# Performance work log

Hardware: AMD Instinct MI355X
Metric: run time of the kernel (lower is better)

The kernel has to match this reference:

```python
import jax, jax.numpy as jnp
import numpy as np

N_UNITS = 100000
N_EDGES = 1600000
NODE_DIM = 64
N_REL_TYPES = 8
LEAKY_SLOPE = 0.2


def setup_inputs() -> dict:
    key = jax.random.key(0)
    k1, k2, k3, k4, k5 = jax.random.split(key, 5)
    x_unit_base = jax.random.normal(k1, (N_UNITS, NODE_DIM), dtype=jnp.float32)
    hat_t = jax.random.normal(k2, (N_UNITS,), dtype=jnp.float32)
    a_r_params = jax.random.normal(k3, (N_REL_TYPES, 2 * NODE_DIM), dtype=jnp.float32)
    rel_edge_index = jax.random.randint(k4, (2, N_EDGES), 0, N_UNITS, dtype=jnp.int64)
    rel_edge_type = jax.random.randint(k5, (N_EDGES,), 0, N_REL_TYPES, dtype=jnp.int64)
    return {
        "x_unit_base": x_unit_base,
        "hat_t": hat_t,
        "a_r_params": a_r_params,
        "rel_edge_index": rel_edge_index,
        "rel_edge_type": rel_edge_type,
    }


def reference(x_unit_base, hat_t, a_r_params, rel_edge_index, rel_edge_type):
    n_units = x_unit_base.shape[0]
    src = rel_edge_index[0]  # [E]
    dst = rel_edge_index[1]  # [E]

    # Per-edge attention params, split into source/dest halves to avoid
    # materializing the [E, 2d] concat explicitly as a separate buffer.
    a_r = a_r_params[rel_edge_type]          # [E, 2d]
    d = x_unit_base.shape[1]
    a_u, a_v = a_r[:, :d], a_r[:, d:]
    # e = sum(a_r * cat(x_u, x_v)) = <a_u, x_u> + <a_v, x_v>
    e = jnp.sum(a_u * x_unit_base[src], axis=-1) + jnp.sum(a_v * x_unit_base[dst], axis=-1)
    e = jax.nn.leaky_relu(e, negative_slope=LEAKY_SLOPE)  # [E]

    # scatter_softmax over edges grouped by src
    seg_max = jax.ops.segment_max(e, src, num_segments=n_units)  # [N]
    ex = jnp.exp(e - seg_max[src])
    denom = jax.ops.segment_sum(ex, src, num_segments=n_units)   # [N]
    alpha = ex / denom[src]                                       # [E]

    # weighted scatter-sum of imputed treatments
    weighted_t = alpha * hat_t[dst]
    g_u = jax.ops.segment_sum(weighted_t, src, num_segments=n_units)  # [N]
    return g_u[:, None]
```

## Files before the change

### kernel.cpp

```cpp
#include <hip/hip_runtime.h>

#define LEAKY_SLOPE 0.2f
#define SHIFT 20.0f
#define CHUNK 2048
#define LG_CHUNK 11
#define NG 8
#define NSL 2
#define NB_MAX 512
#define EPB 4096
#define CAP_MIN 4608


__device__ __forceinline__ float lrelu_exp(float a, float b) {
    float e = a + b;
    e = (e > 0.f) ? e : LEAKY_SLOPE * e;
    return __expf(e - SHIFT);
}

__global__ __launch_bounds__(256) void table_scatter_kernel(
        const float* __restrict__ x, const float* __restrict__ a,
        const float* __restrict__ hat_t,
        const int* __restrict__ src, const int* __restrict__ dst,
        const int* __restrict__ typ,
        float* __restrict__ su, float* __restrict__ svx,
        unsigned* __restrict__ gcur, unsigned* __restrict__ buckets,
        int cap, int nch, int n_units, int n_edges, int gs) {
    __shared__ unsigned lcnt[NB_MAX];
    __shared__ unsigned lbase[NB_MAX];
    const int tid = threadIdx.x;

    if ((int)blockIdx.x < gs) {
        const int nb = nch * NG;
        for (int i = tid; i < nb; i += 256) lcnt[i] = 0u;
        __syncthreads();

        const int base = blockIdx.x * EPB;
        unsigned ent[16], rnk[16], bkt[16];
#pragma unroll
        for (int r = 0; r < 4; ++r) {
            int e = base + tid * 4 + r * 1024;
            if (e + 4 <= n_edges) {
                int4 s4 = *reinterpret_cast<const int4*>(src + e);
                int4 d4 = *reinterpret_cast<const int4*>(dst + e);
                int4 t4 = *reinterpret_cast<const int4*>(typ + e);
                int ss[4] = {s4.x, s4.y, s4.z, s4.w};
                int dd[4] = {d4.x, d4.y, d4.z, d4.w};
                int tt[4] = {t4.x, t4.y, t4.z, t4.w};
#pragma unroll
                for (int i = 0; i < 4; ++i) {
                    unsigned s = (unsigned)ss[i], d = (unsigned)dd[i], t = (unsigned)tt[i];
                    unsigned b = (s >> LG_CHUNK) * NG + ((d >> LG_CHUNK) & (NG - 1));
                    ent[r * 4 + i] = ((s & (CHUNK - 1)) << 21) | (t << 18) | d;
                    bkt[r * 4 + i] = b;
                    rnk[r * 4 + i] = atomicAdd(&lcnt[b], 1u);
                }
            } else {
#pragma unroll
                for (int i = 0; i < 4; ++i) {
                    int ee = e + i;
                    if (ee < n_edges) {
                        unsigned s = (unsigned)src[ee], d = (unsigned)dst[ee], t = (unsigned)typ[ee];
                        unsigned b = (s >> LG_CHUNK) * NG + ((d >> LG_CHUNK) & (NG - 1));
                        ent[r * 4 + i] = ((s & (CHUNK - 1)) << 21) | (t << 18) | d;
                        bkt[r * 4 + i] = b;
                        rnk[r * 4 + i] = atomicAdd(&lcnt[b], 1u);
                    } else {
                        bkt[r * 4 + i] = 0xFFFFFFFFu;
                    }
                }
            }
        }
        __syncthreads();
        for (int i = tid; i < nb; i += 256)
            lbase[i] = lcnt[i] ? atomicAdd(&gcur[i], lcnt[i]) : 0u;
        __syncthreads();
#pragma unroll
        for (int k = 0; k < 16; ++k) {
            unsigned b = bkt[k];
            if (b != 0xFFFFFFFFu) {
                unsigned pos = lbase[b] + rnk[k];
                if (pos < (unsigned)cap)
                    buckets[(size_t)b * cap + pos] = ent[k];
            }
        }
    } else {
        int u = ((int)blockIdx.x - gs) * 256 + tid;
        if (u >= n_units) return;
        float4 xr[16];
        const float4* xp = reinterpret_cast<const float4*>(x + (size_t)u * 64);
#pragma unroll
        for (int k = 0; k < 16; ++k) xr[k] = xp[k];

        float out_u[8], out_v[8];
#pragma unroll
        for (int r = 0; r < 8; ++r) {
            const float* ar = a + r * 128;
            float au = 0.f, av = 0.f;
#pragma unroll
            for (int k = 0; k < 16; ++k) {
                float4 xk = xr[k];
                au = fmaf(ar[4 * k + 0], xk.x, au);
                au = fmaf(ar[4 * k + 1], xk.y, au);
                au = fmaf(ar[4 * k + 2], xk.z, au);
                au = fmaf(ar[4 * k + 3], xk.w, au);
                av = fmaf(ar[64 + 4 * k + 0], xk.x, av);
                av = fmaf(ar[64 + 4 * k + 1], xk.y, av);
                av = fmaf(ar[64 + 4 * k + 2], xk.z, av);
                av = fmaf(ar[64 + 4 * k + 3], xk.w, av);
            }
            out_u[r] = au;
            out_v[r] = av;
        }
        float4* sup = reinterpret_cast<float4*>(su + (size_t)u * 8);
        sup[0] = make_float4(out_u[0], out_u[1], out_u[2], out_u[3]);
        sup[1] = make_float4(out_u[4], out_u[5], out_u[6], out_u[7]);
        float ht = hat_t[u];
        float4* svp = reinterpret_cast<float4*>(svx + (size_t)u * 16);
        svp[0] = make_float4(out_v[0], ht, out_v[1], ht);
        svp[1] = make_float4(out_v[2], ht, out_v[3], ht);
        svp[2] = make_float4(out_v[4], ht, out_v[5], ht);
        svp[3] = make_float4(out_v[6], ht, out_v[7], ht);
    }
}

__device__ __forceinline__ void accum_edge(unsigned e, const float* __restrict__ suc,
                                           const float2* __restrict__ svh,
                                           float* __restrict__ lden,
                                           float* __restrict__ lnum) {
    unsigned s_l = e >> 21;
    unsigned t = (e >> 18) & 7u;
    unsigned d = e & 0x3FFFFu;
    float suv = suc[(s_l << 3) | t];
    float2 pv = svh[((size_t)d << 3) | t];
    float ex = lrelu_exp(suv, pv.x);
    atomicAdd(&lden[s_l], ex);
    atomicAdd(&lnum[s_l], ex * pv.y);
}

__global__ __launch_bounds__(256) void accum_kernel(const unsigned* __restrict__ buckets,
                                                    const unsigned* __restrict__ gcur,
                                                    const float* __restrict__ su,
                                                    const float2* __restrict__ svh,
                                                    float2* __restrict__ partial,
                                                    int cap) {
    __shared__ float lden[CHUNK];
    __shared__ float lnum[CHUNK];
    const int bid = blockIdx.x;
    const int g = bid & (NG - 1);
    const int rest = bid >> 3;
    const int sl = rest & (NSL - 1);
    const int c = rest >> 1;
    for (int i = threadIdx.x; i < CHUNK; i += 256) { lden[i] = 0.f; lnum[i] = 0.f; }
    __syncthreads();

    const int b = c * NG + g;
    int cnt = (int)gcur[b];
    if (cnt > cap) cnt = cap;
    const unsigned* ep = buckets + (size_t)b * cap;
    int lo = (sl * cnt / NSL) & ~3;
    int hi = (sl == NSL - 1) ? cnt : (((sl + 1) * cnt / NSL) & ~3);
    const float* suc = su + (((size_t)c << LG_CHUNK) << 3);

    for (int i = lo + threadIdx.x * 4; i + 4 <= hi; i += 1024) {
        uint4 q = *reinterpret_cast<const uint4*>(ep + i);
        accum_edge(q.x, suc, svh, lden, lnum);
        accum_edge(q.y, suc, svh, lden, lnum);
        accum_edge(q.z, suc, svh, lden, lnum);
        accum_edge(q.w, suc, svh, lden, lnum);
    }
    int rem = (hi - lo) & 3;
    if ((int)threadIdx.x < rem) accum_edge(ep[hi - rem + threadIdx.x], suc, svh, lden, lnum);

    __syncthreads();
    float2* op = partial + (size_t)bid * CHUNK;
    for (int k = threadIdx.x; k < CHUNK; k += 256)
        op[k] = make_float2(lden[k], lnum[k]);
}

__global__ __launch_bounds__(256) void reduce_kernel(const float2* __restrict__ partial,
                                                     float* __restrict__ out,
                                                     int n_units) {
    int u = blockIdx.x * blockDim.x + threadIdx.x;
    if (u >= n_units) return;
    int c = u >> LG_CHUNK;
    int i = u & (CHUNK - 1);
    const float2* p = partial + ((size_t)c * (NSL * NG)) * CHUNK + i;
    float den = 0.f, num = 0.f;
#pragma unroll
    for (int k = 0; k < NSL * NG; ++k) {
        float2 v = p[(size_t)k * CHUNK];
        den += v.x;
        num += v.y;
    }
    out[u] = (den > 0.f) ? num / den : 0.f;
}

template <bool FUSED>
__global__ __launch_bounds__(256) void node_table_fb_kernel(const float* __restrict__ x,
                                                            const float* __restrict__ a,
                                                            const float* __restrict__ hat_t,
                                                            float* __restrict__ su,
                                                            float* __restrict__ svx,
                                                            float2* __restrict__ nd,
                                                            int n_units) {
    int u = blockIdx.x * blockDim.x + threadIdx.x;
    if (u >= n_units) return;
    nd[u] = make_float2(0.f, 0.f);
    float4 xr[16];
    const float4* xp = reinterpret_cast<const float4*>(x + (size_t)u * 64);
#pragma unroll
    for (int k = 0; k < 16; ++k) xr[k] = xp[k];
    float out_u[8], out_v[8];
#pragma unroll
    for (int r = 0; r < 8; ++r) {
        const float* ar = a + r * 128;
        float au = 0.f, av = 0.f;
#pragma unroll
        for (int k = 0; k < 16; ++k) {
            float4 xk = xr[k];
            au = fmaf(ar[4 * k + 0], xk.x, au);
            au = fmaf(ar[4 * k + 1], xk.y, au);
            au = fmaf(ar[4 * k + 2], xk.z, au);
            au = fmaf(ar[4 * k + 3], xk.w, au);
            av = fmaf(ar[64 + 4 * k + 0], xk.x, av);
            av = fmaf(ar[64 + 4 * k + 1], xk.y, av);
            av = fmaf(ar[64 + 4 * k + 2], xk.z, av);
            av = fmaf(ar[64 + 4 * k + 3], xk.w, av);
        }
        out_u[r] = au;
        out_v[r] = av;
    }
    float4* sup = reinterpret_cast<float4*>(su + (size_t)u * 8);
    sup[0] = make_float4(out_u[0], out_u[1], out_u[2], out_u[3]);
    sup[1] = make_float4(out_u[4], out_u[5], out_u[6], out_u[7]);
    if (FUSED) {
        float ht = hat_t[u];
        float4* svp = reinterpret_cast<float4*>(svx + (size_t)u * 16);
        svp[0] = make_float4(out_v[0], ht, out_v[1], ht);
        svp[1] = make_float4(out_v[2], ht, out_v[3], ht);
        svp[2] = make_float4(out_v[4], ht, out_v[5], ht);
        svp[3] = make_float4(out_v[6], ht, out_v[7], ht);
    } else {
        float4* svp = reinterpret_cast<float4*>(svx + (size_t)u * 8);
        svp[0] = make_float4(out_v[0], out_v[1], out_v[2], out_v[3]);
        svp[1] = make_float4(out_v[4], out_v[5], out_v[6], out_v[7]);
    }
}

__device__ __forceinline__ void pair_add_dev(float* f, float a, float b) {
    atomicAdd(f, a);
    atomicAdd(f + 1, b);
}

template <bool FUSED>
__global__ __launch_bounds__(256) void edge_sum_kernel(const int* __restrict__ src,
                                                       const int* __restrict__ dst,
                                                       const int* __restrict__ typ,
                                                       const float* __restrict__ su,
                                                       const float* __restrict__ svx,
                                                       const float* __restrict__ hat_t,
                                                       float2* __restrict__ nd,
                                                       int n_edges) {
    int e0 = (blockIdx.x * blockDim.x + threadIdx.x) * 2;
    float* ndf = (float*)nd;
    if (e0 + 1 < n_edges) {
        int2 s2 = *reinterpret_cast<const int2*>(src + e0);
        int2 d2 = *reinterpret_cast<const int2*>(dst + e0);
        int2 t2 = *reinterpret_cast<const int2*>(typ + e0);
        float su0 = su[(size_t)s2.x * 8 + t2.x];
        float su1 = su[(size_t)s2.y * 8 + t2.y];
        float sv0, sv1, ht0, ht1;
        if (FUSED) {
            const float2* svh = reinterpret_cast<const float2*>(svx);
            float2 p0 = svh[(size_t)d2.x * 8 + t2.x];
            float2 p1 = svh[(size_t)d2.y * 8 + t2.y];
            sv0 = p0.x; ht0 = p0.y;
            sv1 = p1.x; ht1 = p1.y;
        } else {
            sv0 = svx[(size_t)d2.x * 8 + t2.x];
            sv1 = svx[(size_t)d2.y * 8 + t2.y];
            ht0 = hat_t[d2.x];
            ht1 = hat_t[d2.y];
        }
        float ex0 = lrelu_exp(su0, sv0);
        float ex1 = lrelu_exp(su1, sv1);
        pair_add_dev(ndf + 2 * (size_t)s2.x, ex0, ex0 * ht0);
        pair_add_dev(ndf + 2 * (size_t)s2.y, ex1, ex1 * ht1);
    } else if (e0 < n_edges) {
        int s = src[e0], d = dst[e0], t = typ[e0];
        float sv_v, ht;
        if (FUSED) {
            float2 p = reinterpret_cast<const float2*>(svx)[(size_t)d * 8 + t];
            sv_v = p.x; ht = p.y;
        } else {
            sv_v = svx[(size_t)d * 8 + t];
            ht = hat_t[d];
        }
        float ex = lrelu_exp(su[(size_t)s * 8 + t], sv_v);
        pair_add_dev(ndf + 2 * (size_t)s, ex, ex * ht);
    }
}

__global__ __launch_bounds__(256) void finalize_kernel(const float2* __restrict__ nd,
                                                       float* __restrict__ out, int n) {
    int i = blockIdx.x * blockDim.x + threadIdx.x;
    if (i < n) {
        float2 v = nd[i];
        out[i] = (v.x > 0.f) ? v.y / v.x : 0.f;
    }
}

extern "C" void kernel_launch(void* const* d_in, const int* in_sizes, int n_in,
                              void* d_out, int out_size, void* d_ws, size_t ws_size,
                              hipStream_t stream) {
    const float* x     = (const float*)d_in[0];
    const float* hat_t = (const float*)d_in[1];
    const float* a     = (const float*)d_in[2];
    const int*   ei    = (const int*)d_in[3];
    const int*   et    = (const int*)d_in[4];

    const int n_units = in_sizes[1];
    const int n_edges = in_sizes[4];
    const int* src = ei;
    const int* dst = ei + n_edges;

    const size_t n = (size_t)n_units;
    const int B = 256;
    const int gu = (n_units + B - 1) / B;
    char* ws = (char*)d_ws;

    const int nch = (n_units + CHUNK - 1) >> LG_CHUNK;
    const int nb = nch * NG;
    const size_t tab = n * 96;
    const size_t curb = 4096;
    const size_t partb = (size_t)nch * NSL * NG * CHUNK * 8;

    int cap = 0;
    if (nb <= NB_MAX && n_units < (1 << 18)) {
        size_t head = tab + curb + partb;
        if (ws_size > head) {
            cap = (int)((ws_size - head) / ((size_t)nb * 4)) & ~3;
            if (cap > 8192) cap = 8192;
            if (cap < CAP_MIN) cap = 0;
        }
    }

    if (cap > 0) {
        float* su       = (float*)ws;
        float* svx      = su + n * 8;
        unsigned* gcur  = (unsigned*)(ws + tab);
        unsigned* buckets = (unsigned*)(ws + tab + curb);
        float2* partial = (float2*)(ws + tab + curb + (size_t)nb * cap * 4);
        const int gs = (n_edges + EPB - 1) / EPB;

        hipMemsetAsync(gcur, 0, (size_t)nb * 4, stream);
        table_scatter_kernel<<<gs + gu, B, 0, stream>>>(x, a, hat_t, src, dst, et,
                                                        su, svx, gcur, buckets,
                                                        cap, nch, n_units, n_edges, gs);
        accum_kernel<<<nch * NSL * NG, B, 0, stream>>>(buckets, gcur, su,
                                                       (const float2*)svx, partial, cap);
        reduce_kernel<<<gu, B, 0, stream>>>(partial, (float*)d_out, n_units);
    } else if (ws_size >= n * 104) {
        float2* nd = (float2*)ws;
        float* su  = (float*)(ws + n * 8);
        float* svx = su + n * 8;
        const int ge = ((n_edges + 1) / 2 + B - 1) / B;
        node_table_fb_kernel<true><<<gu, B, 0, stream>>>(x, a, hat_t, su, svx, nd, n_units);
        edge_sum_kernel<true><<<ge, B, 0, stream>>>(src, dst, et, su, svx, hat_t, nd, n_edges);
        finalize_kernel<<<gu, B, 0, stream>>>(nd, (float*)d_out, n_units);
    } else {
        float2* nd = (float2*)ws;
        float* su  = (float*)(ws + n * 8);
        float* svx = su + n * 8;
        const int ge = ((n_edges + 1) / 2 + B - 1) / B;
        node_table_fb_kernel<false><<<gu, B, 0, stream>>>(x, a, hat_t, su, svx, nd, n_units);
        edge_sum_kernel<false><<<ge, B, 0, stream>>>(src, dst, et, su, svx, hat_t, nd, n_edges);
        finalize_kernel<<<gu, B, 0, stream>>>(nd, (float*)d_out, n_units);
    }
}
```

Before: 138.3 us.

## Stage bucket scatter through shared memory and drop accum slice split

Result: no change. 137.1 us (-0.9%).

```diff
diff --git a/kernel.cpp b/kernel.cpp
--- a/kernel.cpp
+++ b/kernel.cpp
@@ -5,8 +5,8 @@
 #define CHUNK 2048
 #define LG_CHUNK 11
 #define NG 8
-#define NSL 2
 #define NB_MAX 512
+#define NB_PAD 512
 #define EPB 4096
 #define CAP_MIN 4608
 
@@ -25,13 +25,16 @@
         float* __restrict__ su, float* __restrict__ svx,
         unsigned* __restrict__ gcur, unsigned* __restrict__ buckets,
         int cap, int nch, int n_units, int n_edges, int gs) {
-    __shared__ unsigned lcnt[NB_MAX];
-    __shared__ unsigned lbase[NB_MAX];
+    __shared__ unsigned cnt[NB_PAD];
+    __shared__ unsigned sA[NB_PAD];
+    __shared__ unsigned sB[NB_PAD];
+    __shared__ unsigned sent[EPB];
+    __shared__ unsigned short sbk[EPB];
     const int tid = threadIdx.x;
 
     if ((int)blockIdx.x < gs) {
         const int nb = nch * NG;
-        for (int i = tid; i < nb; i += 256) lcnt[i] = 0u;
+        for (int i = tid; i < NB_PAD; i += 256) cnt[i] = 0u;
         __syncthreads();
 
         const int base = blockIdx.x * EPB;
@@ -52,7 +55,7 @@
                     unsigned b = (s >> LG_CHUNK) * NG + ((d >> LG_CHUNK) & (NG - 1));
                     ent[r * 4 + i] = ((s & (CHUNK - 1)) << 21) | (t << 18) | d;
                     bkt[r * 4 + i] = b;
-                    rnk[r * 4 + i] = atomicAdd(&lcnt[b], 1u);
+                    rnk[r * 4 + i] = atomicAdd(&cnt[b], 1u);
                 }
             } else {
 #pragma unroll
@@ -63,7 +66,7 @@
                         unsigned b = (s >> LG_CHUNK) * NG + ((d >> LG_CHUNK) & (NG - 1));
                         ent[r * 4 + i] = ((s & (CHUNK - 1)) << 21) | (t << 18) | d;
                         bkt[r * 4 + i] = b;
-                        rnk[r * 4 + i] = atomicAdd(&lcnt[b], 1u);
+                        rnk[r * 4 + i] = atomicAdd(&cnt[b], 1u);
                     } else {
                         bkt[r * 4 + i] = 0xFFFFFFFFu;
                     }
@@ -71,17 +74,39 @@
             }
         }
         __syncthreads();
-        for (int i = tid; i < nb; i += 256)
-            lbase[i] = lcnt[i] ? atomicAdd(&gcur[i], lcnt[i]) : 0u;
-        __syncthreads();
+        {
+            for (int i = tid; i < NB_PAD; i += 256)
+                sA[i] = cnt[i] + (i >= 1 ? cnt[i - 1] : 0u);
+            __syncthreads();
+            unsigned* pin = sA;
+            unsigned* pout = sB;
+#pragma unroll
+            for (int off = 2; off < NB_PAD; off <<= 1) {
+                for (int i = tid; i < NB_PAD; i += 256)
+                    pout[i] = pin[i] + (i >= off ? pin[i - off] : 0u);
+                __syncthreads();
+                unsigned* t2 = pin; pin = pout; pout = t2;
+            }
+        }
 #pragma unroll
         for (int k = 0; k < 16; ++k) {
             unsigned b = bkt[k];
             if (b != 0xFFFFFFFFu) {
-                unsigned pos = lbase[b] + rnk[k];
-                if (pos < (unsigned)cap)
-                    buckets[(size_t)b * cap + pos] = ent[k];
+                unsigned slot = (b ? sA[b - 1] : 0u) + rnk[k];
+                sent[slot] = ent[k];
+                sbk[slot] = (unsigned short)b;
             }
+        }
+        __syncthreads();
+        for (int b = tid; b < nb; b += 256)
+            sB[b] = cnt[b] ? atomicAdd(&gcur[b], cnt[b]) : 0u;
+        const int stot = (int)sA[nb - 1];
+        __syncthreads();
+        for (int i = tid; i < stot; i += 256) {
+            unsigned b = sbk[i];
+            unsigned pos = sB[b] + ((unsigned)i - (b ? sA[b - 1] : 0u));
+            if (pos < (unsigned)cap)
+                buckets[(size_t)b * cap + pos] = sent[i];
         }
     } else {
         int u = ((int)blockIdx.x - gs) * 256 + tid;
@@ -147,9 +172,7 @@
     __shared__ float lnum[CHUNK];
     const int bid = blockIdx.x;
     const int g = bid & (NG - 1);
-    const int rest = bid >> 3;
-    const int sl = rest & (NSL - 1);
-    const int c = rest >> 1;
+    const int c = bid >> 3;
     for (int i = threadIdx.x; i < CHUNK; i += 256) { lden[i] = 0.f; lnum[i] = 0.f; }
     __syncthreads();
 
@@ -157,19 +180,17 @@
     int cnt = (int)gcur[b];
     if (cnt > cap) cnt = cap;
     const unsigned* ep = buckets + (size_t)b * cap;
-    int lo = (sl * cnt / NSL) & ~3;
-    int hi = (sl == NSL - 1) ? cnt : (((sl + 1) * cnt / NSL) & ~3);
     const float* suc = su + (((size_t)c << LG_CHUNK) << 3);
 
-    for (int i = lo + threadIdx.x * 4; i + 4 <= hi; i += 1024) {
+    for (int i = threadIdx.x * 4; i + 4 <= cnt; i += 1024) {
         uint4 q = *reinterpret_cast<const uint4*>(ep + i);
         accum_edge(q.x, suc, svh, lden, lnum);
         accum_edge(q.y, suc, svh, lden, lnum);
         accum_edge(q.z, suc, svh, lden, lnum);
         accum_edge(q.w, suc, svh, lden, lnum);
     }
-    int rem = (hi - lo) & 3;
-    if ((int)threadIdx.x < rem) accum_edge(ep[hi - rem + threadIdx.x], suc, svh, lden, lnum);
+    int rem = cnt & 3;
+    if ((int)threadIdx.x < rem) accum_edge(ep[cnt - rem + threadIdx.x], suc, svh, lden, lnum);
 
     __syncthreads();
     float2* op = partial + (size_t)bid * CHUNK;
@@ -184,10 +205,10 @@
     if (u >= n_units) return;
     int c = u >> LG_CHUNK;
     int i = u & (CHUNK - 1);
-    const float2* p = partial + ((size_t)c * (NSL * NG)) * CHUNK + i;
+    const float2* p = partial + ((size_t)c * NG) * CHUNK + i;
     float den = 0.f, num = 0.f;
 #pragma unroll
-    for (int k = 0; k < NSL * NG; ++k) {
+    for (int k = 0; k < NG; ++k) {
         float2 v = p[(size_t)k * CHUNK];
         den += v.x;
         num += v.y;
@@ -333,7 +354,7 @@
     const int nb = nch * NG;
     const size_t tab = n * 96;
     const size_t curb = 4096;
-    const size_t partb = (size_t)nch * NSL * NG * CHUNK * 8;
+    const size_t partb = (size_t)nb * CHUNK * 8;
 
     int cap = 0;
     if (nb <= NB_MAX && n_units < (1 << 18)) {
@@ -357,8 +378,8 @@
         table_scatter_kernel<<<gs + gu, B, 0, stream>>>(x, a, hat_t, src, dst, et,
                                                         su, svx, gcur, buckets,
                                                         cap, nch, n_units, n_edges, gs);
-        accum_kernel<<<nch * NSL * NG, B, 0, stream>>>(buckets, gcur, su,
-                                                       (const float2*)svx, partial, cap);
+        accum_kernel<<<nb, B, 0, stream>>>(buckets, gcur, su,
+                                           (const float2*)svx, partial, cap);
         reduce_kernel<<<gu, B, 0, stream>>>(partial, (float*)d_out, n_units);
     } else if (ws_size >= n * 104) {
         float2* nd = (float2*)ws;
```

## Fuse scatter, accumulate and reduce into one cooperative persistent kernel

Applied to the files above, without the earlier changes.

After: 325.3 us. 2.35x slower.

```diff
diff --git a/kernel.cpp b/kernel.cpp
--- a/kernel.cpp
+++ b/kernel.cpp
@@ -1,4 +1,7 @@
 #include <hip/hip_runtime.h>
+#include <hip/hip_cooperative_groups.h>
+
+namespace cg = cooperative_groups;
 
 #define LEAKY_SLOPE 0.2f
 #define SHIFT 20.0f
@@ -6,7 +9,7 @@
 #define LG_CHUNK 11
 #define NG 8
 #define NSL 2
-#define NB_MAX 512
+#define NB_PAD 512
 #define EPB 4096
 #define CAP_MIN 4608
 
@@ -15,112 +18,6 @@
     float e = a + b;
     e = (e > 0.f) ? e : LEAKY_SLOPE * e;
     return __expf(e - SHIFT);
-}
-
-__global__ __launch_bounds__(256) void table_scatter_kernel(
-        const float* __restrict__ x, const float* __restrict__ a,
-        const float* __restrict__ hat_t,
-        const int* __restrict__ src, const int* __restrict__ dst,
-        const int* __restrict__ typ,
-        float* __restrict__ su, float* __restrict__ svx,
-        unsigned* __restrict__ gcur, unsigned* __restrict__ buckets,
-        int cap, int nch, int n_units, int n_edges, int gs) {
-    __shared__ unsigned lcnt[NB_MAX];
-    __shared__ unsigned lbase[NB_MAX];
-    const int tid = threadIdx.x;
-
-    if ((int)blockIdx.x < gs) {
-        const int nb = nch * NG;
-        for (int i = tid; i < nb; i += 256) lcnt[i] = 0u;
-        __syncthreads();
-
-        const int base = blockIdx.x * EPB;
-        unsigned ent[16], rnk[16], bkt[16];
-#pragma unroll
-        for (int r = 0; r < 4; ++r) {
-            int e = base + tid * 4 + r * 1024;
-            if (e + 4 <= n_edges) {
-                int4 s4 = *reinterpret_cast<const int4*>(src + e);
-                int4 d4 = *reinterpret_cast<const int4*>(dst + e);
-                int4 t4 = *reinterpret_cast<const int4*>(typ + e);
-                int ss[4] = {s4.x, s4.y, s4.z, s4.w};
-                int dd[4] = {d4.x, d4.y, d4.z, d4.w};
-                int tt[4] = {t4.x, t4.y, t4.z, t4.w};
-#pragma unroll
-                for (int i = 0; i < 4; ++i) {
-                    unsigned s = (unsigned)ss[i], d = (unsigned)dd[i], t = (unsigned)tt[i];
-                    unsigned b = (s >> LG_CHUNK) * NG + ((d >> LG_CHUNK) & (NG - 1));
-                    ent[r * 4 + i] = ((s & (CHUNK - 1)) << 21) | (t << 18) | d;
-                    bkt[r * 4 + i] = b;
-                    rnk[r * 4 + i] = atomicAdd(&lcnt[b], 1u);
-                }
-            } else {
-#pragma unroll
-                for (int i = 0; i < 4; ++i) {
-                    int ee = e + i;
-                    if (ee < n_edges) {
-                        unsigned s = (unsigned)src[ee], d = (unsigned)dst[ee], t = (unsigned)typ[ee];
-                        unsigned b = (s >> LG_CHUNK) * NG + ((d >> LG_CHUNK) & (NG - 1));
-                        ent[r * 4 + i] = ((s & (CHUNK - 1)) << 21) | (t << 18) | d;
-                        bkt[r * 4 + i] = b;
-                        rnk[r * 4 + i] = atomicAdd(&lcnt[b], 1u);
-                    } else {
-                        bkt[r * 4 + i] = 0xFFFFFFFFu;
-                    }
-                }
-            }
-        }
-        __syncthreads();
-        for (int i = tid; i < nb; i += 256)
-            lbase[i] = lcnt[i] ? atomicAdd(&gcur[i], lcnt[i]) : 0u;
-        __syncthreads();
-#pragma unroll
-        for (int k = 0; k < 16; ++k) {
-            unsigned b = bkt[k];
-            if (b != 0xFFFFFFFFu) {
-                unsigned pos = lbase[b] + rnk[k];
-                if (pos < (unsigned)cap)
-                    buckets[(size_t)b * cap + pos] = ent[k];
-            }
-        }
-    } else {
-        int u = ((int)blockIdx.x - gs) * 256 + tid;
-        if (u >= n_units) return;
-        float4 xr[16];
-        const float4* xp = reinterpret_cast<const float4*>(x + (size_t)u * 64);
-#pragma unroll
-        for (int k = 0; k < 16; ++k) xr[k] = xp[k];
-
-        float out_u[8], out_v[8];
-#pragma unroll
-        for (int r = 0; r < 8; ++r) {
-            const float* ar = a + r * 128;
-            float au = 0.f, av = 0.f;
-#pragma unroll
-            for (int k = 0; k < 16; ++k) {
-                float4 xk = xr[k];
-                au = fmaf(ar[4 * k + 0], xk.x, au);
-                au = fmaf(ar[4 * k + 1], xk.y, au);
-                au = fmaf(ar[4 * k + 2], xk.z, au);
-                au = fmaf(ar[4 * k + 3], xk.w, au);
-                av = fmaf(ar[64 + 4 * k + 0], xk.x, av);
-                av = fmaf(ar[64 + 4 * k + 1], xk.y, av);
-                av = fmaf(ar[64 + 4 * k + 2], xk.z, av);
-                av = fmaf(ar[64 + 4 * k + 3], xk.w, av);
-            }
-            out_u[r] = au;
-            out_v[r] = av;
-        }
-        float4* sup = reinterpret_cast<float4*>(su + (size_t)u * 8);
-        sup[0] = make_float4(out_u[0], out_u[1], out_u[2], out_u[3]);
-        sup[1] = make_float4(out_u[4], out_u[5], out_u[6], out_u[7]);
-        float ht = hat_t[u];
-        float4* svp = reinterpret_cast<float4*>(svx + (size_t)u * 16);
-        svp[0] = make_float4(out_v[0], ht, out_v[1], ht);
-        svp[1] = make_float4(out_v[2], ht, out_v[3], ht);
-        svp[2] = make_float4(out_v[4], ht, out_v[5], ht);
-        svp[3] = make_float4(out_v[6], ht, out_v[7], ht);
-    }
 }
 
 __device__ __forceinline__ void accum_edge(unsigned e, const float* __restrict__ suc,
@@ -137,62 +34,174 @@
     atomicAdd(&lnum[s_l], ex * pv.y);
 }
 
-__global__ __launch_bounds__(256) void accum_kernel(const unsigned* __restrict__ buckets,
-                                                    const unsigned* __restrict__ gcur,
-                                                    const float* __restrict__ su,
-                                                    const float2* __restrict__ svh,
-                                                    float2* __restrict__ partial,
-                                                    int cap) {
-    __shared__ float lden[CHUNK];
-    __shared__ float lnum[CHUNK];
+__global__ __launch_bounds__(256, 4) void fused_kernel(
+        const float* __restrict__ x, const float* __restrict__ a,
+        const float* __restrict__ hat_t,
+        const int* __restrict__ src, const int* __restrict__ dst,
+        const int* __restrict__ typ,
+        float* __restrict__ su, float* __restrict__ svx,
+        unsigned* __restrict__ gcur, unsigned* __restrict__ buckets,
+        float2* __restrict__ partial, float* __restrict__ out,
+        int cap, int nch, int n_units, int n_edges, int gs, int gu) {
+    __shared__ float lds[2 * CHUNK];
+    cg::grid_group grid = cg::this_grid();
+    const int tid = threadIdx.x;
     const int bid = blockIdx.x;
-    const int g = bid & (NG - 1);
-    const int rest = bid >> 3;
-    const int sl = rest & (NSL - 1);
-    const int c = rest >> 1;
-    for (int i = threadIdx.x; i < CHUNK; i += 256) { lden[i] = 0.f; lnum[i] = 0.f; }
-    __syncthreads();
-
-    const int b = c * NG + g;
-    int cnt = (int)gcur[b];
-    if (cnt > cap) cnt = cap;
-    const unsigned* ep = buckets + (size_t)b * cap;
-    int lo = (sl * cnt / NSL) & ~3;
-    int hi = (sl == NSL - 1) ? cnt : (((sl + 1) * cnt / NSL) & ~3);
-    const float* suc = su + (((size_t)c << LG_CHUNK) << 3);
-
-    for (int i = lo + threadIdx.x * 4; i + 4 <= hi; i += 1024) {
-        uint4 q = *reinterpret_cast<const uint4*>(ep + i);
-        accum_edge(q.x, suc, svh, lden, lnum);
-        accum_edge(q.y, suc, svh, lden, lnum);
-        accum_edge(q.z, suc, svh, lden, lnum);
-        accum_edge(q.w, suc, svh, lden, lnum);
-    }
-    int rem = (hi - lo) & 3;
-    if ((int)threadIdx.x < rem) accum_edge(ep[hi - rem + threadIdx.x], suc, svh, lden, lnum);
-
-    __syncthreads();
-    float2* op = partial + (size_t)bid * CHUNK;
-    for (int k = threadIdx.x; k < CHUNK; k += 256)
-        op[k] = make_float2(lden[k], lnum[k]);
-}
-
-__global__ __launch_bounds__(256) void reduce_kernel(const float2* __restrict__ partial,
-                                                     float* __restrict__ out,
-                                                     int n_units) {
-    int u = blockIdx.x * blockDim.x + threadIdx.x;
-    if (u >= n_units) return;
-    int c = u >> LG_CHUNK;
-    int i = u & (CHUNK - 1);
-    const float2* p = partial + ((size_t)c * (NSL * NG)) * CHUNK + i;
-    float den = 0.f, num = 0.f;
-#pragma unroll
-    for (int k = 0; k < NSL * NG; ++k) {
-        float2 v = p[(size_t)k * CHUNK];
-        den += v.x;
-        num += v.y;
-    }
-    out[u] = (den > 0.f) ? num / den : 0.f;
+    const int G = gridDim.x;
+    const int nb = nch * NG;
+
+    for (int i = bid * 256 + tid; i < nb; i += G * 256) gcur[i] = 0u;
+    grid.sync();
+
+    {
+        unsigned* lcnt = (unsigned*)lds;
+        unsigned* lbase = lcnt + NB_PAD;
+        for (int it = bid; it < gs + gu; it += G) {
+            if (it < gs) {
+                for (int i = tid; i < nb; i += 256) lcnt[i] = 0u;
+                __syncthreads();
+                const int base = it * EPB;
+                unsigned ent[16], rnk[16], bkt[16];
+#pragma unroll
+                for (int r = 0; r < 4; ++r) {
+                    int e = base + tid * 4 + r * 1024;
+                    if (e + 4 <= n_edges) {
+                        int4 s4 = *reinterpret_cast<const int4*>(src + e);
+                        int4 d4 = *reinterpret_cast<const int4*>(dst + e);
+                        int4 t4 = *reinterpret_cast<const int4*>(typ + e);
+                        int ss[4] = {s4.x, s4.y, s4.z, s4.w};
+                        int dd[4] = {d4.x, d4.y, d4.z, d4.w};
+                        int tt[4] = {t4.x, t4.y, t4.z, t4.w};
+#pragma unroll
+                        for (int i = 0; i < 4; ++i) {
+                            unsigned s = (unsigned)ss[i], d = (unsigned)dd[i], t = (unsigned)tt[i];
+                            unsigned b = (s >> LG_CHUNK) * NG + ((d >> LG_CHUNK) & (NG - 1));
+                            ent[r * 4 + i] = ((s & (CHUNK - 1)) << 21) | (t << 18) | d;
+                            bkt[r * 4 + i] = b;
+                            rnk[r * 4 + i] = atomicAdd(&lcnt[b], 1u);
+                        }
+                    } else {
+#pragma unroll
+                        for (int i = 0; i < 4; ++i) {
+                            int ee = e + i;
+                            if (ee < n_edges) {
+                                unsigned s = (unsigned)src[ee], d = (unsigned)dst[ee],
+                                         t = (unsigned)typ[ee];
+                                unsigned b = (s >> LG_CHUNK) * NG + ((d >> LG_CHUNK) & (NG - 1));
+                                ent[r * 4 + i] = ((s & (CHUNK - 1)) << 21) | (t << 18) | d;
+                                bkt[r * 4 + i] = b;
+                                rnk[r * 4 + i] = atomicAdd(&lcnt[b], 1u);
+                            } else {
+                                bkt[r * 4 + i] = 0xFFFFFFFFu;
+                            }
+                        }
+                    }
+                }
+                __syncthreads();
+                for (int i = tid; i < nb; i += 256)
+                    lbase[i] = lcnt[i] ? atomicAdd(&gcur[i], lcnt[i]) : 0u;
+                __syncthreads();
+#pragma unroll
+                for (int k = 0; k < 16; ++k) {
+                    unsigned b = bkt[k];
+                    if (b != 0xFFFFFFFFu) {
+                        unsigned pos = lbase[b] + rnk[k];
+                        if (pos < (unsigned)cap)
+                            buckets[(size_t)b * cap + pos] = ent[k];
+                    }
+                }
+                __syncthreads();
+            } else {
+                int u = (it - gs) * 256 + tid;
+                if (u < n_units) {
+                    float4 xr[16];
+                    const float4* xp = reinterpret_cast<const float4*>(x + (size_t)u * 64);
+#pragma unroll
+                    for (int k = 0; k < 16; ++k) xr[k] = xp[k];
+                    float out_u[8], out_v[8];
+#pragma unroll
+                    for (int r = 0; r < 8; ++r) {
+                        const float* ar = a + r * 128;
+                        float au = 0.f, av = 0.f;
+#pragma unroll
+                        for (int k = 0; k < 16; ++k) {
+                            float4 xk = xr[k];
+                            au = fmaf(ar[4 * k + 0], xk.x, au);
+                            au = fmaf(ar[4 * k + 1], xk.y, au);
+                            au = fmaf(ar[4 * k + 2], xk.z, au);
+                            au = fmaf(ar[4 * k + 3], xk.w, au);
+                            av = fmaf(ar[64 + 4 * k + 0], xk.x, av);
+                            av = fmaf(ar[64 + 4 * k + 1], xk.y, av);
+                            av = fmaf(ar[64 + 4 * k + 2], xk.z, av);
+                            av = fmaf(ar[64 + 4 * k + 3], xk.w, av);
+                        }
+                        out_u[r] = au;
+                        out_v[r] = av;
+                    }
+                    float4* sup = reinterpret_cast<float4*>(su + (size_t)u * 8);
+                    sup[0] = make_float4(out_u[0], out_u[1], out_u[2], out_u[3]);
+                    sup[1] = make_float4(out_u[4], out_u[5], out_u[6], out_u[7]);
+                    float ht = hat_t[u];
+                    float4* svp = reinterpret_cast<float4*>(svx + (size_t)u * 16);
+                    svp[0] = make_float4(out_v[0], ht, out_v[1], ht);
+                    svp[1] = make_float4(out_v[2], ht, out_v[3], ht);
+                    svp[2] = make_float4(out_v[4], ht, out_v[5], ht);
+                    svp[3] = make_float4(out_v[6], ht, out_v[7], ht);
+                }
+            }
+        }
+    }
+    grid.sync();
+
+    {
+        float* lden = lds;
+        float* lnum = lds + CHUNK;
+        const float2* svh = reinterpret_cast<const float2*>(svx);
+        for (int item = bid; item < nb * NSL; item += G) {
+            int g = item & (NG - 1);
+            int rest = item >> 3;
+            int sl = rest & (NSL - 1);
+            int c = rest >> 1;
+            for (int i = tid; i < CHUNK; i += 256) { lden[i] = 0.f; lnum[i] = 0.f; }
+            __syncthreads();
+            const int b = c * NG + g;
+            int cnt = (int)gcur[b];
+            if (cnt > cap) cnt = cap;
+            const unsigned* ep = buckets + (size_t)b * cap;
+            const float* suc = su + (((size_t)c << LG_CHUNK) << 3);
+            int lo = (sl * cnt / NSL) & ~3;
+            int hi = (sl == NSL - 1) ? cnt : (((sl + 1) * cnt / NSL) & ~3);
+            for (int i = lo + tid * 4; i + 4 <= hi; i += 1024) {
+                uint4 q = *reinterpret_cast<const uint4*>(ep + i);
+                accum_edge(q.x, suc, svh, lden, lnum);
+                accum_edge(q.y, suc, svh, lden, lnum);
+                accum_edge(q.z, suc, svh, lden, lnum);
+                accum_edge(q.w, suc, svh, lden, lnum);
+            }
+            int rem = (hi - lo) & 3;
+            if (tid < rem) accum_edge(ep[hi - rem + tid], suc, svh, lden, lnum);
+            __syncthreads();
+            float2* op = partial + (size_t)item * CHUNK;
+            for (int k = tid; k < CHUNK; k += 256)
+                op[k] = make_float2(lden[k], lnum[k]);
+            __syncthreads();
+        }
+    }
+    grid.sync();
+
+    for (int u = bid * 256 + tid; u < n_units; u += G * 256) {
+        int c = u >> LG_CHUNK;
+        int i = u & (CHUNK - 1);
+        const float2* p = partial + ((size_t)c * (NG * NSL)) * CHUNK + i;
+        float den = 0.f, num = 0.f;
+#pragma unroll
+        for (int k = 0; k < NG * NSL; ++k) {
+            float2 v = p[(size_t)k * CHUNK];
+            den += v.x;
+            num += v.y;
+        }
+        out[u] = (den > 0.f) ? num / den : 0.f;
+    }
 }
 
 template <bool FUSED>
@@ -333,10 +342,10 @@
     const int nb = nch * NG;
     const size_t tab = n * 96;
     const size_t curb = 4096;
-    const size_t partb = (size_t)nch * NSL * NG * CHUNK * 8;
+    const size_t partb = (size_t)nb * NSL * CHUNK * 8;
 
     int cap = 0;
-    if (nb <= NB_MAX && n_units < (1 << 18)) {
+    if (nb <= NB_PAD && n_units < (1 << 18)) {
         size_t head = tab + curb + partb;
         if (ws_size > head) {
             cap = (int)((ws_size - head) / ((size_t)nb * 4)) & ~3;
@@ -345,21 +354,34 @@
         }
     }
 
+    int G = 0;
     if (cap > 0) {
+        int dev = 0, ncu = 0, occ = 0;
+        hipGetDevice(&dev);
+        hipDeviceGetAttribute(&ncu, hipDeviceAttributeMultiprocessorCount, dev);
+        hipOccupancyMaxActiveBlocksPerMultiprocessor(&occ, fused_kernel, 256, 0);
+        G = occ * ncu;
+        if (G > 1024) G = 1024;
+        G &= ~7;
+    }
+
+    if (cap > 0 && G >= 8) {
         float* su       = (float*)ws;
         float* svx      = su + n * 8;
         unsigned* gcur  = (unsigned*)(ws + tab);
         unsigned* buckets = (unsigned*)(ws + tab + curb);
         float2* partial = (float2*)(ws + tab + curb + (size_t)nb * cap * 4);
+        float* outp     = (float*)d_out;
         const int gs = (n_edges + EPB - 1) / EPB;
 
-        hipMemsetAsync(gcur, 0, (size_t)nb * 4, stream);
-        table_scatter_kernel<<<gs + gu, B, 0, stream>>>(x, a, hat_t, src, dst, et,
-                                                        su, svx, gcur, buckets,
-                                                        cap, nch, n_units, n_edges, gs);
-        accum_kernel<<<nch * NSL * NG, B, 0, stream>>>(buckets, gcur, su,
-                                                       (const float2*)svx, partial, cap);
-        reduce_kernel<<<gu, B, 0, stream>>>(partial, (float*)d_out, n_units);
+        int nu = n_units, ne = n_edges, gsv = gs, guv = gu, capv = cap, nchv = nch;
+        void* args[] = {(void*)&x, (void*)&a, (void*)&hat_t,
+                        (void*)&src, (void*)&dst, (void*)&et,
+                        (void*)&su, (void*)&svx, (void*)&gcur, (void*)&buckets,
+                        (void*)&partial, (void*)&outp,
+                        (void*)&capv, (void*)&nchv, (void*)&nu, (void*)&ne,
+                        (void*)&gsv, (void*)&guv};
+        hipLaunchCooperativeKernel((void*)fused_kernel, dim3(G), dim3(B), args, 0, stream);
     } else if (ws_size >= n * 104) {
         float2* nd = (float2*)ws;
         float* su  = (float*)(ws + n * 8);
```

## Bucket edges by small source chunks and fuse accumulation with final division

Applied to the files above, without the earlier changes.

Measured after the change: 134.6 us, median of 2. 1.03x faster.

```diff
diff --git a/kernel.cpp b/kernel.cpp
--- a/kernel.cpp
+++ b/kernel.cpp
@@ -2,13 +2,10 @@
 
 #define LEAKY_SLOPE 0.2f
 #define SHIFT 20.0f
-#define CHUNK 2048
-#define LG_CHUNK 11
-#define NG 8
-#define NSL 2
-#define NB_MAX 512
+#define CHUNK 128
+#define LG_CHUNK 7
+#define NB_MAX 1024
 #define EPB 4096
-#define CAP_MIN 4608
 
 
 __device__ __forceinline__ float lrelu_exp(float a, float b) {
@@ -19,18 +16,16 @@
 
 __global__ __launch_bounds__(256) void table_scatter_kernel(
         const float* __restrict__ x, const float* __restrict__ a,
-        const float* __restrict__ hat_t,
         const int* __restrict__ src, const int* __restrict__ dst,
         const int* __restrict__ typ,
-        float* __restrict__ su, float* __restrict__ svx,
+        float* __restrict__ su, float* __restrict__ sv,
         unsigned* __restrict__ gcur, unsigned* __restrict__ buckets,
-        int cap, int nch, int n_units, int n_edges, int gs) {
-    __shared__ unsigned lcnt[NB_MAX];
-    __shared__ unsigned lbase[NB_MAX];
+        int cap, int nb, int n_units, int n_edges, int gs) {
     const int tid = threadIdx.x;
 
     if ((int)blockIdx.x < gs) {
-        const int nb = nch * NG;
+        __shared__ unsigned lcnt[NB_MAX];
+        __shared__ unsigned lbase[NB_MAX];
         for (int i = tid; i < nb; i += 256) lcnt[i] = 0u;
         __syncthreads();
 
@@ -49,7 +44,7 @@
 #pragma unroll
                 for (int i = 0; i < 4; ++i) {
                     unsigned s = (unsigned)ss[i], d = (unsigned)dd[i], t = (unsigned)tt[i];
-                    unsigned b = (s >> LG_CHUNK) * NG + ((d >> LG_CHUNK) & (NG - 1));
+                    unsigned b = s >> LG_CHUNK;
                     ent[r * 4 + i] = ((s & (CHUNK - 1)) << 21) | (t << 18) | d;
                     bkt[r * 4 + i] = b;
                     rnk[r * 4 + i] = atomicAdd(&lcnt[b], 1u);
@@ -59,8 +54,9 @@
                 for (int i = 0; i < 4; ++i) {
                     int ee = e + i;
                     if (ee < n_edges) {
-                        unsigned s = (unsigned)src[ee], d = (unsigned)dst[ee], t = (unsigned)typ[ee];
-                        unsigned b = (s >> LG_CHUNK) * NG + ((d >> LG_CHUNK) & (NG - 1));
+                        unsigned s = (unsigned)src[ee], d = (unsigned)dst[ee],
+                                 t = (unsigned)typ[ee];
+                        unsigned b = s >> LG_CHUNK;
                         ent[r * 4 + i] = ((s & (CHUNK - 1)) << 21) | (t << 18) | d;
                         bkt[r * 4 + i] = b;
                         rnk[r * 4 + i] = atomicAdd(&lcnt[b], 1u);
@@ -114,85 +110,61 @@
         float4* sup = reinterpret_cast<float4*>(su + (size_t)u * 8);
         sup[0] = make_float4(out_u[0], out_u[1], out_u[2], out_u[3]);
         sup[1] = make_float4(out_u[4], out_u[5], out_u[6], out_u[7]);
-        float ht = hat_t[u];
-        float4* svp = reinterpret_cast<float4*>(svx + (size_t)u * 16);
-        svp[0] = make_float4(out_v[0], ht, out_v[1], ht);
-        svp[1] = make_float4(out_v[2], ht, out_v[3], ht);
-        svp[2] = make_float4(out_v[4], ht, out_v[5], ht);
-        svp[3] = make_float4(out_v[6], ht, out_v[7], ht);
+        float4* svp = reinterpret_cast<float4*>(sv + (size_t)u * 8);
+        svp[0] = make_float4(out_v[0], out_v[1], out_v[2], out_v[3]);
+        svp[1] = make_float4(out_v[4], out_v[5], out_v[6], out_v[7]);
     }
 }
 
 __device__ __forceinline__ void accum_edge(unsigned e, const float* __restrict__ suc,
-                                           const float2* __restrict__ svh,
+                                           const float* __restrict__ sv,
+                                           const float* __restrict__ hat_t,
                                            float* __restrict__ lden,
                                            float* __restrict__ lnum) {
     unsigned s_l = e >> 21;
     unsigned t = (e >> 18) & 7u;
     unsigned d = e & 0x3FFFFu;
     float suv = suc[(s_l << 3) | t];
-    float2 pv = svh[((size_t)d << 3) | t];
-    float ex = lrelu_exp(suv, pv.x);
+    float svv = sv[((size_t)d << 3) | t];
+    float ht = hat_t[d];
+    float ex = lrelu_exp(suv, svv);
     atomicAdd(&lden[s_l], ex);
-    atomicAdd(&lnum[s_l], ex * pv.y);
-}
-
-__global__ __launch_bounds__(256) void accum_kernel(const unsigned* __restrict__ buckets,
-                                                    const unsigned* __restrict__ gcur,
-                                                    const float* __restrict__ su,
-                                                    const float2* __restrict__ svh,
-                                                    float2* __restrict__ partial,
-                                                    int cap) {
+    atomicAdd(&lnum[s_l], ex * ht);
+}
+
+__global__ __launch_bounds__(256) void accum_final_kernel(
+        const unsigned* __restrict__ buckets, const unsigned* __restrict__ gcur,
+        const float* __restrict__ su, const float* __restrict__ sv,
+        const float* __restrict__ hat_t, float* __restrict__ out,
+        int cap, int n_units) {
     __shared__ float lden[CHUNK];
     __shared__ float lnum[CHUNK];
-    const int bid = blockIdx.x;
-    const int g = bid & (NG - 1);
-    const int rest = bid >> 3;
-    const int sl = rest & (NSL - 1);
-    const int c = rest >> 1;
-    for (int i = threadIdx.x; i < CHUNK; i += 256) { lden[i] = 0.f; lnum[i] = 0.f; }
+    const int c = blockIdx.x;
+    const int tid = threadIdx.x;
+    if (tid < CHUNK) { lden[tid] = 0.f; lnum[tid] = 0.f; }
     __syncthreads();
 
-    const int b = c * NG + g;
-    int cnt = (int)gcur[b];
+    int cnt = (int)gcur[c];
     if (cnt > cap) cnt = cap;
-    const unsigned* ep = buckets + (size_t)b * cap;
-    int lo = (sl * cnt / NSL) & ~3;
-    int hi = (sl == NSL - 1) ? cnt : (((sl + 1) * cnt / NSL) & ~3);
+    const unsigned* ep = buckets + (size_t)c * cap;
     const float* suc = su + (((size_t)c << LG_CHUNK) << 3);
 
-    for (int i = lo + threadIdx.x * 4; i + 4 <= hi; i += 1024) {
+    for (int i = tid * 4; i + 4 <= cnt; i += 1024) {
         uint4 q = *reinterpret_cast<const uint4*>(ep + i);
-        accum_edge(q.x, suc, svh, lden, lnum);
-        accum_edge(q.y, suc, svh, lden, lnum);
-        accum_edge(q.z, suc, svh, lden, lnum);
-        accum_edge(q.w, suc, svh, lden, lnum);
-    }
-    int rem = (hi - lo) & 3;
-    if ((int)threadIdx.x < rem) accum_edge(ep[hi - rem + threadIdx.x], suc, svh, lden, lnum);
+        accum_edge(q.x, suc, sv, hat_t, lden, lnum);
+        accum_edge(q.y, suc, sv, hat_t, lden, lnum);
+        accum_edge(q.z, suc, sv, hat_t, lden, lnum);
+        accum_edge(q.w, suc, sv, hat_t, lden, lnum);
+    }
+    int rem = cnt & 3;
+    if (tid < rem) accum_edge(ep[cnt - rem + tid], suc, sv, hat_t, lden, lnum);
 
     __syncthreads();
-    float2* op = partial + (size_t)bid * CHUNK;
-    for (int k = threadIdx.x; k < CHUNK; k += 256)
-        op[k] = make_float2(lden[k], lnum[k]);
-}
-
-__global__ __launch_bounds__(256) void reduce_kernel(const float2* __restrict__ partial,
-                                                     float* __restrict__ out,
-                                                     int n_units) {
-    int u = blockIdx.x * blockDim.x + threadIdx.x;
-    if (u >= n_units) return;
-    int c = u >> LG_CHUNK;
-    int i = u & (CHUNK - 1);
-    const float2* p = partial + ((size_t)c * (NSL * NG)) * CHUNK + i;
-    float den = 0.f, num = 0.f;
-#pragma unroll
-    for (int k = 0; k < NSL * NG; ++k) {
-        float2 v = p[(size_t)k * CHUNK];
-        den += v.x;
-        num += v.y;
-    }
-    out[u] = (den > 0.f) ? num / den : 0.f;
+    int u = (c << LG_CHUNK) + tid;
+    if (tid < CHUNK && u < n_units) {
+        float den = lden[tid];
+        out[u] = (den > 0.f) ? lnum[tid] / den : 0.f;
+    }
 }
 
 template <bool FUSED>
@@ -329,37 +301,34 @@
     const int gu = (n_units + B - 1) / B;
     char* ws = (char*)d_ws;
 
-    const int nch = (n_units + CHUNK - 1) >> LG_CHUNK;
-    const int nb = nch * NG;
-    const size_t tab = n * 96;
-    const size_t curb = 4096;
-    const size_t partb = (size_t)nch * NSL * NG * CHUNK * 8;
+    const int nb = (n_units + CHUNK - 1) >> LG_CHUNK;
+    const size_t tab = n * 64;
+    const size_t curb = ((size_t)nb * 4 + 255) & ~255;
 
     int cap = 0;
     if (nb <= NB_MAX && n_units < (1 << 18)) {
-        size_t head = tab + curb + partb;
+        double mean = (double)n_edges / nb;
+        int cap_min = ((int)(mean + 8.0 * __builtin_sqrt(mean) + 16.0) + 3) & ~3;
+        size_t head = tab + curb;
         if (ws_size > head) {
-            cap = (int)((ws_size - head) / ((size_t)nb * 4)) & ~3;
-            if (cap > 8192) cap = 8192;
-            if (cap < CAP_MIN) cap = 0;
+            int cmax = (int)((ws_size - head) / ((size_t)nb * 4)) & ~3;
+            if (cmax >= cap_min) cap = cap_min;
         }
     }
 
     if (cap > 0) {
-        float* su       = (float*)ws;
-        float* svx      = su + n * 8;
-        unsigned* gcur  = (unsigned*)(ws + tab);
+        float* su        = (float*)ws;
+        float* sv        = su + n * 8;
+        unsigned* gcur   = (unsigned*)(ws + tab);
         unsigned* buckets = (unsigned*)(ws + tab + curb);
-        float2* partial = (float2*)(ws + tab + curb + (size_t)nb * cap * 4);
         const int gs = (n_edges + EPB - 1) / EPB;
 
         hipMemsetAsync(gcur, 0, (size_t)nb * 4, stream);
-        table_scatter_kernel<<<gs + gu, B, 0, stream>>>(x, a, hat_t, src, dst, et,
-                                                        su, svx, gcur, buckets,
-                                                        cap, nch, n_units, n_edges, gs);
-        accum_kernel<<<nch * NSL * NG, B, 0, stream>>>(buckets, gcur, su,
-                                                       (const float2*)svx, partial, cap);
-        reduce_kernel<<<gu, B, 0, stream>>>(partial, (float*)d_out, n_units);
+        table_scatter_kernel<<<gs + gu, B, 0, stream>>>(x, a, src, dst, et,
+                                                        su, sv, gcur, buckets,
+                                                        cap, nb, n_units, n_edges, gs);
+        accum_final_kernel<<<nb, B, 0, stream>>>(buckets, gcur, su, sv, hat_t,
+                                                 (float*)d_out, cap, n_units);
     } else if (ws_size >= n * 104) {
         float2* nd = (float2*)ws;
         float* su  = (float*)(ws + n * 8);
```
